# Kernel optimization log

Hardware: AMD Instinct MI355X
Metric: run time of the kernel (lower is better)

Reference implementation:

```python
import jax, jax.numpy as jnp
import numpy as np

# graph metadata: 3 node types, 4 canonical etypes
NT_SRC = (0, 1, 1, 2)   # src ntype of each relation
NT_DST = (1, 0, 2, 1)   # dst ntype of each relation
GROUPS = {0: (1,), 1: (0, 3), 2: (2,)}  # relations sharing each dst ntype (in dict order)
NEG_SLOPE = 0.2
N_NODES, N_EDGES, IN_DIM = 50000, 200000, 256
HEADS, HID = 8, 32
REL_IN, REL_HID = 64, 32


def _leaky(x):
    return jax.nn.leaky_relu(x, NEG_SLOPE)


def _segment_softmax(e, seg, n):
    # numerically stable softmax over edges grouped by dst node
    m = jax.ops.segment_max(e, seg, num_segments=n)
    ex = jnp.exp(e - m[seg])
    s = jax.ops.segment_sum(ex, seg, num_segments=n)
    return ex / s[seg]


def setup_inputs() -> dict:
    key = jax.random.key(0)
    ks = jax.random.split(key, 12)
    w = 0.05  # xavier-like scale
    feat = jax.random.normal(ks[0], (4, N_NODES, IN_DIM), jnp.float32)
    rel_emb = jax.random.normal(ks[1], (4, REL_IN), jnp.float32)
    node_W = jax.random.normal(ks[2], (3, IN_DIM, HEADS * HID), jnp.float32) * w
    rel_W = jax.random.normal(ks[3], (4, REL_IN, HEADS * 2 * HID), jnp.float32) * w
    res_W = jax.random.normal(ks[4], (3, IN_DIM, HEADS * HID), jnp.float32) * w
    res_b = jnp.zeros((3, HEADS * HID), jnp.float32)
    res_alpha = jax.random.normal(ks[5], (3,), jnp.float32)
    cross_attn = jax.random.normal(ks[6], (4, HEADS, HID), jnp.float32) * w
    prop_W = jax.random.normal(ks[7], (4, REL_IN, HEADS * REL_HID), jnp.float32) * w
    prop_b = jnp.zeros((4, HEADS * REL_HID), jnp.float32)
    src_idx = jax.random.randint(ks[8], (4, N_EDGES), 0, N_NODES, jnp.int32)
    dst_idx = jax.random.randint(ks[9], (4, N_EDGES), 0, N_NODES, jnp.int32)
    return dict(feat=feat, rel_emb=rel_emb, node_W=node_W, rel_W=rel_W,
                res_W=res_W, res_b=res_b, res_alpha=res_alpha,
                cross_attn=cross_attn, prop_W=prop_W, prop_b=prop_b,
                src_idx=src_idx, dst_idx=dst_idx)


def reference(feat, rel_emb, node_W, rel_W, res_W, res_b, res_alpha,
              cross_attn, prop_W, prop_b, src_idx, dst_idx):
    R, N, _ = feat.shape
    H, D = HEADS, HID
    conv_out = []
    for r in range(R):  # fixed small set of relations
        s, d = NT_SRC[r], NT_DST[r]
        # RelationGraphConv (dropout is identity in eval)
        fsrc = (feat[r] @ node_W[s]).reshape(N, H, D)
        fdst = (feat[r] @ node_W[d]).reshape(N, H, D)
        ra = (rel_emb[r] @ rel_W[r]).reshape(H, 2 * D)
        e_dst = (fdst * ra[:, :D]).sum(-1)           # (N, H)
        e_src = (fsrc * ra[:, D:]).sum(-1)           # (N, H)
        e = _leaky(e_src[src_idx[r]] + e_dst[dst_idx[r]])  # (E, H)
        a = _segment_softmax(e, dst_idx[r], N)       # edge softmax per dst node
        msg = fsrc[src_idx[r]] * a[:, :, None]       # (E, H, D)
        out = jax.ops.segment_sum(msg, dst_idx[r], num_segments=N)
        out = jax.nn.relu(out.reshape(N, H * D))
        # residual gate
        alpha = jax.nn.sigmoid(res_alpha[d])
        out = out * alpha + (feat[r] @ res_W[d] + res_b[d]) * (1.0 - alpha)
        conv_out.append(out)
    # RelationCrossing over relations sharing the dst ntype
    node_out = []
    for r in range(R):
        group = GROUPS[NT_DST[r]]
        if len(group) == 1:
            node_out.append(conv_out[group[0]])
        else:
            stacked = jnp.stack([conv_out[g] for g in group], 0).reshape(len(group), N, H, D)
            att = _leaky((stacked * cross_attn[r]).sum(-1, keepdims=True))  # (Rg, N, H, 1)
            att = jax.nn.softmax(att, axis=0)
            node_out.append((stacked * att).sum(0).reshape(N, H * D))
    node_out = jnp.stack(node_out, 0)                # (4, N, H*D)
    # relation embedding propagation
    rel_out = jnp.einsum('ri,rio->ro', rel_emb, prop_W) + prop_b  # (4, H*rel_hid)
    return node_out, rel_out
```

## Files before the change

kernel.cpp:

```cpp
#include <hip/hip_runtime.h>
#include <hip/hip_bf16.h>
#include <stdint.h>

typedef unsigned int u32;
typedef unsigned short u16;
typedef short short8 __attribute__((ext_vector_type(8)));
typedef float f32x4 __attribute__((ext_vector_type(4)));
typedef unsigned short u16x4 __attribute__((ext_vector_type(4)));
typedef __attribute__((address_space(1))) const u32 gu32;
typedef __attribute__((address_space(3))) u32 lu32;

#define NN 50000
#define NE 200000
#define WCT 576

__device__ __forceinline__ float leaky(float x){ return x >= 0.f ? x : 0.2f*x; }
__device__ __forceinline__ float bf2f(u16 u){ return __uint_as_float(((u32)u)<<16); }
__device__ __forceinline__ u16 f2bf(float f){
    u32 u = __float_as_uint(f);
    u32 r = (u + 0x7fffu + ((u>>16)&1u)) >> 16;
    return (u16)r;
}
__device__ __forceinline__ u32 pack_bf2(float a, float b){
    return __builtin_amdgcn_perm(__float_as_uint(b), __float_as_uint(a), 0x07060302u);
}
__device__ __forceinline__ int nt_src(int r){ return (r==0)?0:((r==3)?2:1); }
__device__ __forceinline__ int nt_dst(int r){ return (r==1)?0:((r==2)?2:1); }

__global__ void k_ra(const float* __restrict__ rel_emb, const float* __restrict__ rel_W,
                     float* __restrict__ ra){
    int r = blockIdx.x;
    for (int j = threadIdx.x; j < 512; j += blockDim.x){
        float acc = 0.f;
        for (int i = 0; i < 64; i++) acc += rel_emb[r*64+i] * rel_W[(r*64+i)*512 + j];
        ra[r*512 + j] = acc;
    }
}

__global__ void k_wcat(const float* __restrict__ node_W, const float* __restrict__ res_W,
                       const float* __restrict__ ra, u16* __restrict__ WcatS){
    int g = blockIdx.x*blockDim.x + threadIdx.x;
    if (g >= 4*WCT*256) return;
    int r = g/147456; int rem = g%147456;
    int tile = rem/16384; int rem2 = rem%16384;
    int kc = rem2/512; int rem3 = rem2%512;
    int nrow = rem3>>3; int off = rem3&7;
    int n = tile*64 + nrow;
    int k = kc*8 + off;
    int s = nt_src(r), d = nt_dst(r);
    float v;
    if (n < 256) v = node_W[(s*256+k)*256 + n];
    else if (n < 512) v = res_W[(d*256+k)*256 + (n-256)];
    else if (n < 520){
        int h = n-512; float a = 0.f;
        for (int dd = 0; dd < 32; dd++) a += node_W[(s*256+k)*256 + h*32+dd] * ra[r*512 + h*64+32+dd];
        v = a;
    } else if (n < 528){
        int h = n-520; float a = 0.f;
        for (int dd = 0; dd < 32; dd++) a += node_W[(d*256+k)*256 + h*32+dd] * ra[r*512 + h*64+dd];
        v = a;
    } else v = 0.f;
    WcatS[g] = f2bf(v);
}

__launch_bounds__(512, 4)
__global__ void k_gemm(const float* __restrict__ feat, const u16* __restrict__ WcatS,
                       const float* __restrict__ res_b,
                       u16* __restrict__ fsrc, u16* __restrict__ resb,
                       float* __restrict__ e_comb){
    __shared__ uint4 lsB[4096];
    const short8* lsB8 = (const short8*)lsB;

    int r = blockIdx.y;
    int row0 = blockIdx.x*128;
    const float* A = feat + (size_t)r*NN*256;
    const u16*   W = WcatS + (size_t)r*9*16384;

    int t = threadIdx.x;
    int w = t>>6, l = t&63;
    int wm = (w>>1)*32, wn = (w&1)*32;
    int li = l & 15, lg = l >> 4;

    short8 afr[2][8];
    #pragma unroll
    for (int mt = 0; mt < 2; mt++){
        int grow = row0 + wm + mt*16 + li; if (grow > NN-1) grow = NN-1;
        const float* ap = A + (size_t)grow*256 + lg*8;
        #pragma unroll
        for (int kk = 0; kk < 8; kk++){
            f32x4 x = __builtin_nontemporal_load((const f32x4*)(ap + kk*32));
            f32x4 y = __builtin_nontemporal_load((const f32x4*)(ap + kk*32 + 4));
            short8 f;
            ((u32*)&f)[0] = pack_bf2(x.x, x.y);
            ((u32*)&f)[1] = pack_bf2(x.z, x.w);
            ((u32*)&f)[2] = pack_bf2(y.x, y.y);
            ((u32*)&f)[3] = pack_bf2(y.z, y.w);
            afr[mt][kk] = f;
        }
    }

    #pragma unroll
    for (int i = 0; i < 4; i++){
        int chunk = i*512 + t;
        __builtin_amdgcn_global_load_lds((gu32*)(W + (size_t)chunk*8),
                                         (lu32*)((char*)lsB + chunk*16), 16, 0, 0);
    }
    __syncthreads();

    int d = nt_dst(r);
    int orow = t>>2, oq = t&3;
    int ogrow = row0 + orow;
    size_t onidx = (size_t)r*NN + ogrow;

    for (int T = 0; T < 8; T++){
        int cur = T & 1;
        {
            const u16* tb = W + (size_t)(T+1)*16384;
            char* lb = (char*)lsB + (cur^1)*32768;
            #pragma unroll
            for (int i = 0; i < 4; i++){
                int chunk = i*512 + t;
                __builtin_amdgcn_global_load_lds((gu32*)(tb + (size_t)chunk*8),
                                                 (lu32*)(lb + chunk*16), 16, 0, 0);
            }
        }
        f32x4 acc[2][2] = {};
        #pragma unroll
        for (int kk = 0; kk < 8; kk++){
            short8 bfr[2];
            #pragma unroll
            for (int nt = 0; nt < 2; nt++)
                bfr[nt] = lsB8[cur*2048 + (kk*4+lg)*64 + wn + nt*16 + li];
            #pragma unroll
            for (int mt = 0; mt < 2; mt++)
                #pragma unroll
                for (int nt = 0; nt < 2; nt++)
                    acc[mt][nt] = __builtin_amdgcn_mfma_f32_16x16x32_bf16(afr[mt][kk], bfr[nt], acc[mt][nt], 0,0,0);
        }
        float bias[2] = {0.f, 0.f};
        if (T >= 4){
            bias[0] = res_b[d*256 + (T-4)*64 + wn + li];
            bias[1] = res_b[d*256 + (T-4)*64 + wn + 16 + li];
        }
        __syncthreads();
        u16* cst = (u16*)(lsB + (size_t)cur*2048);
        #pragma unroll
        for (int mt = 0; mt < 2; mt++)
            #pragma unroll
            for (int nt = 0; nt < 2; nt++)
                #pragma unroll
                for (int qq = 0; qq < 4; qq++)
                    cst[(wm + mt*16 + lg*4 + qq)*72 + wn + nt*16 + li] = f2bf(acc[mt][nt][qq] + bias[nt]);
        __syncthreads();
        if (ogrow < NN){
            u16* dst = (T < 4) ? (fsrc + onidx*256 + T*64) : (resb + onidx*256 + (T-4)*64);
            const uint4* src = (const uint4*)(cst + orow*72 + oq*16);
            uint4* dq = (uint4*)(dst + oq*16);
            dq[0] = src[0];
            dq[1] = src[1];
        }
        __syncthreads();
    }

    if (wn == 0){
        f32x4 acc[2] = {};
        #pragma unroll
        for (int kk = 0; kk < 8; kk++){
            short8 bfr = lsB8[(kk*4+lg)*64 + li];
            #pragma unroll
            for (int mt = 0; mt < 2; mt++)
                acc[mt] = __builtin_amdgcn_mfma_f32_16x16x32_bf16(afr[mt][kk], bfr, acc[mt], 0,0,0);
        }
        #pragma unroll
        for (int mt = 0; mt < 2; mt++)
            #pragma unroll
            for (int qq = 0; qq < 4; qq++){
                int row = row0 + wm + mt*16 + lg*4 + qq;
                if (row < NN)
                    e_comb[((size_t)r*NN + row)*16 + li] = acc[mt][qq];
            }
    }
}


__global__ void k_count(const int* __restrict__ dst_idx, u32* __restrict__ cnt){
    int r = blockIdx.y; int e = blockIdx.x*256 + threadIdx.x;
    if (e >= NE) return;
    atomicAdd(&cnt[r*NN + dst_idx[r*NE+e]], 1u);
}

__global__ void k_scan1(const u32* __restrict__ cnt, u32* __restrict__ bsum){
    int r = blockIdx.y, b = blockIdx.x;
    int i = b*256 + threadIdx.x;
    u32 v = (i < NN) ? cnt[r*NN+i] : 0u;
    #pragma unroll
    for (int off = 1; off < 64; off <<= 1) v += __shfl_xor(v, off, 64);
    __shared__ u32 wsum[4];
    int lane = threadIdx.x & 63, w = threadIdx.x >> 6;
    if (lane == 0) wsum[w] = v;
    __syncthreads();
    if (threadIdx.x == 0) bsum[r*256 + b] = wsum[0]+wsum[1]+wsum[2]+wsum[3];
}

__device__ __forceinline__ u32 block_scan_incl(u32 v){
    __shared__ u32 wsum[4];
    int lane = threadIdx.x & 63, w = threadIdx.x >> 6;
    #pragma unroll
    for (int off = 1; off < 64; off <<= 1){
        u32 t = __shfl_up(v, off, 64);
        if (lane >= off) v += t;
    }
    if (lane == 63) wsum[w] = v;
    __syncthreads();
    u32 add = 0;
    #pragma unroll
    for (int k = 0; k < 4; k++) if (k < w) add += wsum[k];
    return v + add;
}

__global__ void k_scan2(u32* __restrict__ bsum){
    int r = blockIdx.x;
    u32 v = bsum[r*256 + threadIdx.x];
    u32 incl = block_scan_incl(v);
    bsum[r*256 + threadIdx.x] = incl - v;
}

__global__ void k_scan3(const u32* __restrict__ cnt, const u32* __restrict__ bsum,
                        u32* __restrict__ row_ptr){
    int r = blockIdx.y, b = blockIdx.x;
    int i = b*256 + threadIdx.x;
    u32 v = (i < NN) ? cnt[r*NN+i] : 0u;
    u32 incl = block_scan_incl(v);
    if (i < NN) row_ptr[r*(NN+1) + i + 1] = bsum[r*256 + b] + incl;
    if (b == 0 && threadIdx.x == 0) row_ptr[r*(NN+1)] = 0u;
}

__global__ void k_scatter(const int* __restrict__ src_idx, const int* __restrict__ dst_idx,
                          const float* __restrict__ e_comb,
                          const u32* __restrict__ row_ptr, u32* __restrict__ cnt2,
                          u32* __restrict__ src_pack, float* __restrict__ e_pack){
    int r = blockIdx.y; int e = blockIdx.x*256 + threadIdx.x;
    if (e >= NE) return;
    int s = src_idx[r*NE+e], d = dst_idx[r*NE+e];
    u32 pos = row_ptr[r*(NN+1)+d] + atomicAdd(&cnt2[r*NN+d], 1u);
    src_pack[r*NE + pos] = (u32)s;
    const f32x4* es = (const f32x4*)(e_comb + (size_t)(r*NN+s)*16);
    const f32x4* ed = (const f32x4*)(e_comb + (size_t)(r*NN+d)*16 + 8);
    f32x4 s0 = es[0], s1 = es[1], d0 = ed[0], d1 = ed[1];
    f32x4 w0, w1;
    w0.x = __expf(leaky(s0.x+d0.x)); w0.y = __expf(leaky(s0.y+d0.y));
    w0.z = __expf(leaky(s0.z+d0.z)); w0.w = __expf(leaky(s0.w+d0.w));
    w1.x = __expf(leaky(s1.x+d1.x)); w1.y = __expf(leaky(s1.y+d1.y));
    w1.z = __expf(leaky(s1.z+d1.z)); w1.w = __expf(leaky(s1.w+d1.w));
    f32x4* ep = (f32x4*)(e_pack + ((size_t)(r*NE)+pos)*8);
    ep[0] = w0; ep[1] = w1;
}

__device__ __forceinline__ void agg_core(int n, int r, int l, int h,
                                         const u32* __restrict__ row_ptr,
                                         const u32* __restrict__ src_pack,
                                         const float* __restrict__ e_pack,
                                         const u16* __restrict__ fsrc,
                                         const u16* __restrict__ resb,
                                         const float* __restrict__ res_alpha,
                                         float& c0, float& c1, float& c2, float& c3){
    u32 p0 = row_ptr[r*(NN+1)+n];
    u32 p1 = row_ptr[r*(NN+1)+n+1];
    int deg = (int)(p1 - p0);

    float s = 0.f;
    for (int i = (l>>3); i < deg; i += 8)
        s += e_pack[((size_t)(r*NE) + p0 + i)*8 + (l&7)];
    #pragma unroll
    for (int msk = 8; msk < 64; msk <<= 1)
        s += __shfl_xor(s, msk, 64);
    float sh = __shfl(s, h, 64);
    float inv_sh = (deg > 0) ? 1.0f / sh : 0.f;

    float a0=0.f, a1=0.f, a2=0.f, a3=0.f;
    const size_t ebase = (size_t)r*NE + p0;
    const u16* fbase = fsrc + (size_t)r*NN*256;
    for (int base = 0; base < deg; base += 64){
        int rem = deg - base; if (rem > 64) rem = 64;
        u32 my_src = 0;
        if (l < rem) my_src = src_pack[ebase + base + l];
        int i = 0;
        for (; i+4 <= rem; i += 4){
            u32 s0 = __shfl(my_src, i, 64);
            u32 s1 = __shfl(my_src, i+1, 64);
            u32 s2 = __shfl(my_src, i+2, 64);
            u32 s3 = __shfl(my_src, i+3, 64);
            float ex0 = e_pack[(ebase + base + i)*8 + h];
            float ex1 = e_pack[(ebase + base + i + 1)*8 + h];
            float ex2 = e_pack[(ebase + base + i + 2)*8 + h];
            float ex3 = e_pack[(ebase + base + i + 3)*8 + h];
            ushort4 f0 = *(const ushort4*)(fbase + (size_t)s0*256 + l*4);
            ushort4 f1 = *(const ushort4*)(fbase + (size_t)s1*256 + l*4);
            ushort4 f2 = *(const ushort4*)(fbase + (size_t)s2*256 + l*4);
            ushort4 f3 = *(const ushort4*)(fbase + (size_t)s3*256 + l*4);
            float w0 = ex0*inv_sh, w1 = ex1*inv_sh, w2 = ex2*inv_sh, w3 = ex3*inv_sh;
            a0 += bf2f(f0.x)*w0 + bf2f(f1.x)*w1 + bf2f(f2.x)*w2 + bf2f(f3.x)*w3;
            a1 += bf2f(f0.y)*w0 + bf2f(f1.y)*w1 + bf2f(f2.y)*w2 + bf2f(f3.y)*w3;
            a2 += bf2f(f0.z)*w0 + bf2f(f1.z)*w1 + bf2f(f2.z)*w2 + bf2f(f3.z)*w3;
            a3 += bf2f(f0.w)*w0 + bf2f(f1.w)*w1 + bf2f(f2.w)*w2 + bf2f(f3.w)*w3;
        }
        for (; i < rem; i++){
            u32 s0 = __shfl(my_src, i, 64);
            float w0 = e_pack[(ebase + base + i)*8 + h]*inv_sh;
            ushort4 f0 = *(const ushort4*)(fbase + (size_t)s0*256 + l*4);
            a0 += bf2f(f0.x)*w0; a1 += bf2f(f0.y)*w0; a2 += bf2f(f0.z)*w0; a3 += bf2f(f0.w)*w0;
        }
    }

    int d = nt_dst(r);
    float alpha = 1.f/(1.f + __expf(-res_alpha[d]));
    float beta = 1.f - alpha;
    u16x4 rv = __builtin_nontemporal_load((const u16x4*)(resb + ((size_t)r*NN+n)*256 + l*4));
    c0 = fmaxf(a0,0.f)*alpha + bf2f(rv.x)*beta;
    c1 = fmaxf(a1,0.f)*alpha + bf2f(rv.y)*beta;
    c2 = fmaxf(a2,0.f)*alpha + bf2f(rv.z)*beta;
    c3 = fmaxf(a3,0.f)*alpha + bf2f(rv.w)*beta;
}

__launch_bounds__(128)
__global__ void k_agg12(const u32* __restrict__ row_ptr, const u32* __restrict__ src_pack,
                        const float* __restrict__ e_pack, const u16* __restrict__ fsrc,
                        const u16* __restrict__ resb, const float* __restrict__ res_alpha,
                        float* __restrict__ out){
    int n = blockIdx.x;
    int r = 1 + (threadIdx.x >> 6);
    int l = threadIdx.x & 63;
    int h = l >> 3;
    float c0, c1, c2, c3;
    agg_core(n, r, l, h, row_ptr, src_pack, e_pack, fsrc, resb, res_alpha, c0, c1, c2, c3);
    f32x4 o = {c0, c1, c2, c3};
    __builtin_nontemporal_store(o, (f32x4*)(out + ((size_t)r*NN+n)*256 + l*4));
}

__launch_bounds__(128)
__global__ void k_aggx03(const u32* __restrict__ row_ptr, const u32* __restrict__ src_pack,
                         const float* __restrict__ e_pack, const u16* __restrict__ fsrc,
                         const u16* __restrict__ resb, const float* __restrict__ res_alpha,
                         const float* __restrict__ cross_attn, float* __restrict__ out){
    __shared__ float cbuf[2][256];
    __shared__ float dots[4][8];

    int n = blockIdx.x;
    int w = threadIdx.x >> 6;
    int r = w ? 3 : 0;
    int l = threadIdx.x & 63;
    int h = l >> 3;
    float c0, c1, c2, c3;
    agg_core(n, r, l, h, row_ptr, src_pack, e_pack, fsrc, resb, res_alpha, c0, c1, c2, c3);

    int slot = w;
    cbuf[slot][l*4+0] = c0; cbuf[slot][l*4+1] = c1;
    cbuf[slot][l*4+2] = c2; cbuf[slot][l*4+3] = c3;
    const float* ca0 = cross_attn;
    const float* ca3 = cross_attn + 3*256;
    float d0 = c0*ca0[l*4+0] + c1*ca0[l*4+1] + c2*ca0[l*4+2] + c3*ca0[l*4+3];
    float d3 = c0*ca3[l*4+0] + c1*ca3[l*4+1] + c2*ca3[l*4+2] + c3*ca3[l*4+3];
    #pragma unroll
    for (int msk = 1; msk < 8; msk <<= 1){
        d0 += __shfl_xor(d0, msk, 64);
        d3 += __shfl_xor(d3, msk, 64);
    }
    if ((l & 7) == 0){
        dots[slot*2+0][h] = d0;
        dots[slot*2+1][h] = d3;
    }
    __syncthreads();
    float g0 = (r == 0) ? dots[0][h] : dots[1][h];
    float g3 = (r == 0) ? dots[2][h] : dots[3][h];
    g0 = leaky(g0); g3 = leaky(g3);
    float mm = fmaxf(g0, g3);
    float w0 = __expf(g0-mm), w3 = __expf(g3-mm);
    float inv = 1.f/(w0+w3);
    w0 *= inv; w3 *= inv;
    f32x4 o;
    o.x = w0*cbuf[0][l*4+0] + w3*cbuf[1][l*4+0];
    o.y = w0*cbuf[0][l*4+1] + w3*cbuf[1][l*4+1];
    o.z = w0*cbuf[0][l*4+2] + w3*cbuf[1][l*4+2];
    o.w = w0*cbuf[0][l*4+3] + w3*cbuf[1][l*4+3];
    __builtin_nontemporal_store(o, (f32x4*)(out + ((size_t)r*NN+n)*256 + l*4));
}

__global__ void k_relout(const float* __restrict__ rel_emb, const float* __restrict__ prop_W,
                         const float* __restrict__ prop_b, float* __restrict__ out){
    int r = blockIdx.x; int o = threadIdx.x;
    float acc = prop_b[r*256 + o];
    for (int i = 0; i < 64; i++) acc += rel_emb[r*64+i] * prop_W[(r*64+i)*256 + o];
    out[(size_t)4*NN*256 + r*256 + o] = acc;
}

extern "C" void kernel_launch(void* const* d_in, const int* in_sizes, int n_in,
                              void* d_out, int out_size, void* d_ws, size_t ws_size,
                              hipStream_t stream){
    const float* feat      = (const float*)d_in[0];
    const float* rel_emb   = (const float*)d_in[1];
    const float* node_W    = (const float*)d_in[2];
    const float* rel_W     = (const float*)d_in[3];
    const float* res_W     = (const float*)d_in[4];
    const float* res_b     = (const float*)d_in[5];
    const float* res_alpha = (const float*)d_in[6];
    const float* cross_attn= (const float*)d_in[7];
    const float* prop_W    = (const float*)d_in[8];
    const float* prop_b    = (const float*)d_in[9];
    const int* src_idx     = (const int*)d_in[10];
    const int* dst_idx     = (const int*)d_in[11];
    float* out = (float*)d_out;

    char* ws = (char*)d_ws;
    u32*   cnt     = (u32*)  (ws);
    u32*   cnt2    = (u32*)  (ws + 800000);
    u32*   bsum    = (u32*)  (ws + 1600000);
    u32*   row_ptr = (u32*)  (ws + 1604096);
    float* ra      = (float*)(ws + 2404112);
    u16*   WcatS   = (u16*)  (ws + 2412304);
    float* e_comb  = (float*)(ws + 3591952);
    u32*   src_pack= (u32*)  (ws + 16391952);
    float* e_pack  = (float*)(ws + 19591952);
    u16*   fsrc    = (u16*)  (ws + 45191952);
    u16*   resb    = (u16*)  (ws + 147591952);

    hipMemsetAsync(cnt, 0, 1604096, stream);

    k_ra<<<4, 256, 0, stream>>>(rel_emb, rel_W, ra);
    k_wcat<<<(4*WCT*256)/256, 256, 0, stream>>>(node_W, res_W, ra, WcatS);
    dim3 gg((NN+127)/128, 4);
    k_gemm<<<gg, 512, 0, stream>>>(feat, WcatS, res_b, fsrc, resb, e_comb);

    dim3 geg((NE+255)/256, 4);
    k_count<<<geg, 256, 0, stream>>>(dst_idx, cnt);
    dim3 gsc((NN+255)/256, 4);
    k_scan1<<<gsc, 256, 0, stream>>>(cnt, bsum);
    k_scan2<<<4, 256, 0, stream>>>(bsum);
    k_scan3<<<gsc, 256, 0, stream>>>(cnt, bsum, row_ptr);
    k_scatter<<<geg, 256, 0, stream>>>(src_idx, dst_idx, e_comb, row_ptr, cnt2,
                                       src_pack, e_pack);
    k_agg12<<<NN, 128, 0, stream>>>(row_ptr, src_pack, e_pack, fsrc, resb,
                                    res_alpha, out);
    k_aggx03<<<NN, 128, 0, stream>>>(row_ptr, src_pack, e_pack, fsrc, resb,
                                     res_alpha, cross_attn, out);
    k_relout<<<4, 256, 0, stream>>>(rel_emb, prop_W, prop_b, out);
}
```

Baseline: 428.1 us.

## Split aggregation into per-relation launches and store GEMM outputs directly

Aggregation now runs as one launch per relation, with four destination nodes per 256-thread block, instead of mixing two relations per 128-thread block. This keeps each relation's gathered feature table hot in cache and removes the LDS exchange and barrier from the cross-relation step. Relation 0's result goes to a bf16 scratch buffer that reuses relation 1's freed fsrc slot, and the final kernel mixes it with relation 3. That adds an extra write and read and bf16 rounding of an intermediate. Separately, the GEMM epilogue writes bf16 results straight to global memory rather than staging them through LDS, which drops two barriers per tile but makes the stores narrower and strided.

```diff
diff --git a/kernel.cpp b/kernel.cpp
--- a/kernel.cpp
+++ b/kernel.cpp
@@ -108,10 +108,6 @@
     __syncthreads();
 
     int d = nt_dst(r);
-    int orow = t>>2, oq = t&3;
-    int ogrow = row0 + orow;
-    size_t onidx = (size_t)r*NN + ogrow;
-
     for (int T = 0; T < 8; T++){
         int cur = T & 1;
         {
@@ -143,23 +139,19 @@
             bias[1] = res_b[d*256 + (T-4)*64 + wn + 16 + li];
         }
         __syncthreads();
-        u16* cst = (u16*)(lsB + (size_t)cur*2048);
+        u16* base = (T < 4) ? fsrc : resb;
+        int cb = (T & 3)*64 + wn;
         #pragma unroll
         for (int mt = 0; mt < 2; mt++)
             #pragma unroll
-            for (int nt = 0; nt < 2; nt++)
-                #pragma unroll
-                for (int qq = 0; qq < 4; qq++)
-                    cst[(wm + mt*16 + lg*4 + qq)*72 + wn + nt*16 + li] = f2bf(acc[mt][nt][qq] + bias[nt]);
-        __syncthreads();
-        if (ogrow < NN){
-            u16* dst = (T < 4) ? (fsrc + onidx*256 + T*64) : (resb + onidx*256 + (T-4)*64);
-            const uint4* src = (const uint4*)(cst + orow*72 + oq*16);
-            uint4* dq = (uint4*)(dst + oq*16);
-            dq[0] = src[0];
-            dq[1] = src[1];
-        }
-        __syncthreads();
+            for (int qq = 0; qq < 4; qq++){
+                int row = row0 + wm + mt*16 + lg*4 + qq;
+                if (row < NN){
+                    size_t off = ((size_t)r*NN + row)*256 + cb;
+                    base[off + li]      = f2bf(acc[mt][0][qq] + bias[0]);
+                    base[off + 16 + li] = f2bf(acc[mt][1][qq] + bias[1]);
+                }
+            }
     }
 
     if (wn == 0){
@@ -322,67 +314,76 @@
     c3 = fmaxf(a3,0.f)*alpha + bf2f(rv.w)*beta;
 }
 
-__launch_bounds__(128)
-__global__ void k_agg12(const u32* __restrict__ row_ptr, const u32* __restrict__ src_pack,
-                        const float* __restrict__ e_pack, const u16* __restrict__ fsrc,
-                        const u16* __restrict__ resb, const float* __restrict__ res_alpha,
-                        float* __restrict__ out){
-    int n = blockIdx.x;
-    int r = 1 + (threadIdx.x >> 6);
+__launch_bounds__(256)
+__global__ void k_aggr(const u32* __restrict__ row_ptr, const u32* __restrict__ src_pack,
+                       const float* __restrict__ e_pack, const u16* __restrict__ fsrc,
+                       const u16* __restrict__ resb, const float* __restrict__ res_alpha,
+                       float* __restrict__ out, int r){
+    int n = blockIdx.x*4 + (threadIdx.x >> 6);
+    if (n >= NN) return;
+    int l = threadIdx.x & 63;
+    float c0, c1, c2, c3;
+    agg_core(n, r, l, l>>3, row_ptr, src_pack, e_pack, fsrc, resb, res_alpha, c0, c1, c2, c3);
+    f32x4 o = {c0, c1, c2, c3};
+    __builtin_nontemporal_store(o, (f32x4*)(out + ((size_t)r*NN+n)*256 + l*4));
+}
+
+__launch_bounds__(256)
+__global__ void k_aggA(const u32* __restrict__ row_ptr, const u32* __restrict__ src_pack,
+                       const float* __restrict__ e_pack, const u16* __restrict__ fsrc,
+                       const u16* __restrict__ resb, const float* __restrict__ res_alpha,
+                       u16* __restrict__ tmp0){
+    int n = blockIdx.x*4 + (threadIdx.x >> 6);
+    if (n >= NN) return;
+    int l = threadIdx.x & 63;
+    float c0, c1, c2, c3;
+    agg_core(n, 0, l, l>>3, row_ptr, src_pack, e_pack, fsrc, resb, res_alpha, c0, c1, c2, c3);
+    u16x4 o = {f2bf(c0), f2bf(c1), f2bf(c2), f2bf(c3)};
+    *(u16x4*)(tmp0 + (size_t)n*256 + l*4) = o;
+}
+
+__launch_bounds__(256)
+__global__ void k_aggB(const u32* __restrict__ row_ptr, const u32* __restrict__ src_pack,
+                       const float* __restrict__ e_pack, const u16* __restrict__ fsrc,
+                       const u16* __restrict__ resb, const float* __restrict__ res_alpha,
+                       const u16* __restrict__ tmp0, const float* __restrict__ cross_attn,
+                       float* __restrict__ out){
+    int n = blockIdx.x*4 + (threadIdx.x >> 6);
+    if (n >= NN) return;
     int l = threadIdx.x & 63;
     int h = l >> 3;
-    float c0, c1, c2, c3;
-    agg_core(n, r, l, h, row_ptr, src_pack, e_pack, fsrc, resb, res_alpha, c0, c1, c2, c3);
-    f32x4 o = {c0, c1, c2, c3};
-    __builtin_nontemporal_store(o, (f32x4*)(out + ((size_t)r*NN+n)*256 + l*4));
-}
-
-__launch_bounds__(128)
-__global__ void k_aggx03(const u32* __restrict__ row_ptr, const u32* __restrict__ src_pack,
-                         const float* __restrict__ e_pack, const u16* __restrict__ fsrc,
-                         const u16* __restrict__ resb, const float* __restrict__ res_alpha,
-                         const float* __restrict__ cross_attn, float* __restrict__ out){
-    __shared__ float cbuf[2][256];
-    __shared__ float dots[4][8];
-
-    int n = blockIdx.x;
-    int w = threadIdx.x >> 6;
-    int r = w ? 3 : 0;
-    int l = threadIdx.x & 63;
-    int h = l >> 3;
-    float c0, c1, c2, c3;
-    agg_core(n, r, l, h, row_ptr, src_pack, e_pack, fsrc, resb, res_alpha, c0, c1, c2, c3);
-
-    int slot = w;
-    cbuf[slot][l*4+0] = c0; cbuf[slot][l*4+1] = c1;
-    cbuf[slot][l*4+2] = c2; cbuf[slot][l*4+3] = c3;
+    float b0, b1, b2, b3;
+    agg_core(n, 3, l, h, row_ptr, src_pack, e_pack, fsrc, resb, res_alpha, b0, b1, b2, b3);
+    u16x4 tv = *(const u16x4*)(tmp0 + (size_t)n*256 + l*4);
+    float a0 = bf2f(tv.x), a1 = bf2f(tv.y), a2 = bf2f(tv.z), a3 = bf2f(tv.w);
+
     const float* ca0 = cross_attn;
     const float* ca3 = cross_attn + 3*256;
-    float d0 = c0*ca0[l*4+0] + c1*ca0[l*4+1] + c2*ca0[l*4+2] + c3*ca0[l*4+3];
-    float d3 = c0*ca3[l*4+0] + c1*ca3[l*4+1] + c2*ca3[l*4+2] + c3*ca3[l*4+3];
+    float w00 = a0*ca0[l*4+0] + a1*ca0[l*4+1] + a2*ca0[l*4+2] + a3*ca0[l*4+3];
+    float w30 = b0*ca0[l*4+0] + b1*ca0[l*4+1] + b2*ca0[l*4+2] + b3*ca0[l*4+3];
+    float w03 = a0*ca3[l*4+0] + a1*ca3[l*4+1] + a2*ca3[l*4+2] + a3*ca3[l*4+3];
+    float w33 = b0*ca3[l*4+0] + b1*ca3[l*4+1] + b2*ca3[l*4+2] + b3*ca3[l*4+3];
     #pragma unroll
     for (int msk = 1; msk < 8; msk <<= 1){
-        d0 += __shfl_xor(d0, msk, 64);
-        d3 += __shfl_xor(d3, msk, 64);
-    }
-    if ((l & 7) == 0){
-        dots[slot*2+0][h] = d0;
-        dots[slot*2+1][h] = d3;
-    }
-    __syncthreads();
-    float g0 = (r == 0) ? dots[0][h] : dots[1][h];
-    float g3 = (r == 0) ? dots[2][h] : dots[3][h];
-    g0 = leaky(g0); g3 = leaky(g3);
+        w00 += __shfl_xor(w00, msk, 64);
+        w30 += __shfl_xor(w30, msk, 64);
+        w03 += __shfl_xor(w03, msk, 64);
+        w33 += __shfl_xor(w33, msk, 64);
+    }
+    float g0 = leaky(w00), g3 = leaky(w30);
     float mm = fmaxf(g0, g3);
-    float w0 = __expf(g0-mm), w3 = __expf(g3-mm);
-    float inv = 1.f/(w0+w3);
-    w0 *= inv; w3 *= inv;
-    f32x4 o;
-    o.x = w0*cbuf[0][l*4+0] + w3*cbuf[1][l*4+0];
-    o.y = w0*cbuf[0][l*4+1] + w3*cbuf[1][l*4+1];
-    o.z = w0*cbuf[0][l*4+2] + w3*cbuf[1][l*4+2];
-    o.w = w0*cbuf[0][l*4+3] + w3*cbuf[1][l*4+3];
-    __builtin_nontemporal_store(o, (f32x4*)(out + ((size_t)r*NN+n)*256 + l*4));
+    float e0 = __expf(g0-mm), e3 = __expf(g3-mm);
+    float inv = 1.f/(e0+e3);
+    float u0 = e0*inv, u3 = e3*inv;
+    f32x4 o0 = {u0*a0 + u3*b0, u0*a1 + u3*b1, u0*a2 + u3*b2, u0*a3 + u3*b3};
+    __builtin_nontemporal_store(o0, (f32x4*)(out + (size_t)n*256 + l*4));
+    float q0 = leaky(w03), q3 = leaky(w33);
+    float mq = fmaxf(q0, q3);
+    float v0 = __expf(q0-mq), v3 = __expf(q3-mq);
+    float iv = 1.f/(v0+v3);
+    v0 *= iv; v3 *= iv;
+    f32x4 o3 = {v0*a0 + v3*b0, v0*a1 + v3*b1, v0*a2 + v3*b2, v0*a3 + v3*b3};
+    __builtin_nontemporal_store(o3, (f32x4*)(out + ((size_t)3*NN+n)*256 + l*4));
 }
 
 __global__ void k_relout(const float* __restrict__ rel_emb, const float* __restrict__ prop_W,
@@ -422,6 +423,7 @@
     float* e_pack  = (float*)(ws + 19591952);
     u16*   fsrc    = (u16*)  (ws + 45191952);
     u16*   resb    = (u16*)  (ws + 147591952);
+    u16*   tmp0    = fsrc + (size_t)NN*256;
 
     hipMemsetAsync(cnt, 0, 1604096, stream);
 
@@ -438,9 +440,11 @@
     k_scan3<<<gsc, 256, 0, stream>>>(cnt, bsum, row_ptr);
     k_scatter<<<geg, 256, 0, stream>>>(src_idx, dst_idx, e_comb, row_ptr, cnt2,
                                        src_pack, e_pack);
-    k_agg12<<<NN, 128, 0, stream>>>(row_ptr, src_pack, e_pack, fsrc, resb,
-                                    res_alpha, out);
-    k_aggx03<<<NN, 128, 0, stream>>>(row_ptr, src_pack, e_pack, fsrc, resb,
-                                     res_alpha, cross_attn, out);
+    int gag = (NN+3)/4;
+    k_aggr<<<gag, 256, 0, stream>>>(row_ptr, src_pack, e_pack, fsrc, resb, res_alpha, out, 1);
+    k_aggr<<<gag, 256, 0, stream>>>(row_ptr, src_pack, e_pack, fsrc, resb, res_alpha, out, 2);
+    k_aggA<<<gag, 256, 0, stream>>>(row_ptr, src_pack, e_pack, fsrc, resb, res_alpha, tmp0);
+    k_aggB<<<gag, 256, 0, stream>>>(row_ptr, src_pack, e_pack, fsrc, resb, res_alpha,
+                                    tmp0, cross_attn, out);
     k_relout<<<4, 256, 0, stream>>>(rel_emb, prop_W, prop_b, out);
 }
```

Measured after the change: 453.8 us. +6.0%, slower.

## Write GEMM outputs directly from registers and pad node stride to remove syncs

Applied to the files above, without the earlier changes.

The GEMM epilogue no longer stages bf16 results through LDS with three block barriers per tile. Each lane now stores its accumulator values straight to global memory, using a padded per-relation row stride (NNP) so the bounds checks can go. The first weight tile load is issued before the A-fragment loads, biases are preloaded once, and the T loop is unrolled with manual vmcnt waits and a single barrier per iteration. In exchange, global stores become narrow 2-byte scattered writes instead of coalesced 16-byte rows, and the workspace layout grows. Correctness also depends on the hand-tuned s_waitcnt counts.

```diff
diff --git a/kernel.cpp b/kernel.cpp
--- a/kernel.cpp
+++ b/kernel.cpp
@@ -11,6 +11,7 @@
 typedef __attribute__((address_space(3))) u32 lu32;
 
 #define NN 50000
+#define NNP 50048
 #define NE 200000
 #define WCT 576
 
@@ -81,6 +82,13 @@
     int wm = (w>>1)*32, wn = (w&1)*32;
     int li = l & 15, lg = l >> 4;
 
+    #pragma unroll
+    for (int i = 0; i < 4; i++){
+        int chunk = i*512 + t;
+        __builtin_amdgcn_global_load_lds((gu32*)(W + (size_t)chunk*8),
+                                         (lu32*)((char*)lsB + chunk*16), 16, 0, 0);
+    }
+
     short8 afr[2][8];
     #pragma unroll
     for (int mt = 0; mt < 2; mt++){
@@ -99,19 +107,20 @@
         }
     }
 
-    #pragma unroll
-    for (int i = 0; i < 4; i++){
-        int chunk = i*512 + t;
-        __builtin_amdgcn_global_load_lds((gu32*)(W + (size_t)chunk*8),
-                                         (lu32*)((char*)lsB + chunk*16), 16, 0, 0);
-    }
-    __syncthreads();
-
     int d = nt_dst(r);
-    int orow = t>>2, oq = t&3;
-    int ogrow = row0 + orow;
-    size_t onidx = (size_t)r*NN + ogrow;
-
+    float bias0[4], bias1[4];
+    #pragma unroll
+    for (int j = 0; j < 4; j++){
+        bias0[j] = res_b[d*256 + j*64 + wn + li];
+        bias1[j] = res_b[d*256 + j*64 + wn + 16 + li];
+        asm volatile("" : "+v"(bias0[j]), "+v"(bias1[j]));
+    }
+
+    asm volatile("s_waitcnt vmcnt(0)" ::: "memory");
+    __builtin_amdgcn_sched_barrier(0);
+    __builtin_amdgcn_s_barrier();
+
+    #pragma unroll
     for (int T = 0; T < 8; T++){
         int cur = T & 1;
         {
@@ -124,6 +133,7 @@
                                                  (lu32*)(lb + chunk*16), 16, 0, 0);
             }
         }
+        __builtin_amdgcn_sched_barrier(0);
         f32x4 acc[2][2] = {};
         #pragma unroll
         for (int kk = 0; kk < 8; kk++){
@@ -137,29 +147,22 @@
                 for (int nt = 0; nt < 2; nt++)
                     acc[mt][nt] = __builtin_amdgcn_mfma_f32_16x16x32_bf16(afr[mt][kk], bfr[nt], acc[mt][nt], 0,0,0);
         }
-        float bias[2] = {0.f, 0.f};
-        if (T >= 4){
-            bias[0] = res_b[d*256 + (T-4)*64 + wn + li];
-            bias[1] = res_b[d*256 + (T-4)*64 + wn + 16 + li];
-        }
-        __syncthreads();
-        u16* cst = (u16*)(lsB + (size_t)cur*2048);
+        u16* base = (T < 4) ? fsrc : resb;
+        int cb = (T & 3)*64 + wn;
+        float b0 = (T >= 4) ? bias0[T-4] : 0.f;
+        float b1 = (T >= 4) ? bias1[T-4] : 0.f;
         #pragma unroll
         for (int mt = 0; mt < 2; mt++)
             #pragma unroll
-            for (int nt = 0; nt < 2; nt++)
-                #pragma unroll
-                for (int qq = 0; qq < 4; qq++)
-                    cst[(wm + mt*16 + lg*4 + qq)*72 + wn + nt*16 + li] = f2bf(acc[mt][nt][qq] + bias[nt]);
-        __syncthreads();
-        if (ogrow < NN){
-            u16* dst = (T < 4) ? (fsrc + onidx*256 + T*64) : (resb + onidx*256 + (T-4)*64);
-            const uint4* src = (const uint4*)(cst + orow*72 + oq*16);
-            uint4* dq = (uint4*)(dst + oq*16);
-            dq[0] = src[0];
-            dq[1] = src[1];
-        }
-        __syncthreads();
+            for (int qq = 0; qq < 4; qq++){
+                int row = row0 + wm + mt*16 + lg*4 + qq;
+                size_t off = ((size_t)r*NNP + row)*256 + cb;
+                base[off + li]      = f2bf(acc[mt][0][qq] + b0);
+                base[off + 16 + li] = f2bf(acc[mt][1][qq] + b1);
+            }
+        asm volatile("s_waitcnt vmcnt(16)" ::: "memory");
+        __builtin_amdgcn_sched_barrier(0);
+        __builtin_amdgcn_s_barrier();
     }
 
     if (wn == 0){
@@ -176,8 +179,7 @@
             #pragma unroll
             for (int qq = 0; qq < 4; qq++){
                 int row = row0 + wm + mt*16 + lg*4 + qq;
-                if (row < NN)
-                    e_comb[((size_t)r*NN + row)*16 + li] = acc[mt][qq];
+                e_comb[((size_t)r*NNP + row)*16 + li] = acc[mt][qq];
             }
     }
 }
@@ -244,8 +246,8 @@
     int s = src_idx[r*NE+e], d = dst_idx[r*NE+e];
     u32 pos = row_ptr[r*(NN+1)+d] + atomicAdd(&cnt2[r*NN+d], 1u);
     src_pack[r*NE + pos] = (u32)s;
-    const f32x4* es = (const f32x4*)(e_comb + (size_t)(r*NN+s)*16);
-    const f32x4* ed = (const f32x4*)(e_comb + (size_t)(r*NN+d)*16 + 8);
+    const f32x4* es = (const f32x4*)(e_comb + ((size_t)r*NNP + s)*16);
+    const f32x4* ed = (const f32x4*)(e_comb + ((size_t)r*NNP + d)*16 + 8);
     f32x4 s0 = es[0], s1 = es[1], d0 = ed[0], d1 = ed[1];
     f32x4 w0, w1;
     w0.x = __expf(leaky(s0.x+d0.x)); w0.y = __expf(leaky(s0.y+d0.y));
@@ -279,7 +281,7 @@
 
     float a0=0.f, a1=0.f, a2=0.f, a3=0.f;
     const size_t ebase = (size_t)r*NE + p0;
-    const u16* fbase = fsrc + (size_t)r*NN*256;
+    const u16* fbase = fsrc + (size_t)r*NNP*256;
     for (int base = 0; base < deg; base += 64){
         int rem = deg - base; if (rem > 64) rem = 64;
         u32 my_src = 0;
@@ -315,7 +317,7 @@
     int d = nt_dst(r);
     float alpha = 1.f/(1.f + __expf(-res_alpha[d]));
     float beta = 1.f - alpha;
-    u16x4 rv = __builtin_nontemporal_load((const u16x4*)(resb + ((size_t)r*NN+n)*256 + l*4));
+    u16x4 rv = __builtin_nontemporal_load((const u16x4*)(resb + ((size_t)r*NNP+n)*256 + l*4));
     c0 = fmaxf(a0,0.f)*alpha + bf2f(rv.x)*beta;
     c1 = fmaxf(a1,0.f)*alpha + bf2f(rv.y)*beta;
     c2 = fmaxf(a2,0.f)*alpha + bf2f(rv.z)*beta;
@@ -418,16 +420,16 @@
     float* ra      = (float*)(ws + 2404112);
     u16*   WcatS   = (u16*)  (ws + 2412304);
     float* e_comb  = (float*)(ws + 3591952);
-    u32*   src_pack= (u32*)  (ws + 16391952);
-    float* e_pack  = (float*)(ws + 19591952);
-    u16*   fsrc    = (u16*)  (ws + 45191952);
-    u16*   resb    = (u16*)  (ws + 147591952);
+    u32*   src_pack= (u32*)  (ws + 16404240);
+    float* e_pack  = (float*)(ws + 19604240);
+    u16*   fsrc    = (u16*)  (ws + 45204240);
+    u16*   resb    = (u16*)  (ws + 147702544);
 
     hipMemsetAsync(cnt, 0, 1604096, stream);
 
     k_ra<<<4, 256, 0, stream>>>(rel_emb, rel_W, ra);
     k_wcat<<<(4*WCT*256)/256, 256, 0, stream>>>(node_W, res_W, ra, WcatS);
-    dim3 gg((NN+127)/128, 4);
+    dim3 gg(NNP/128, 4);
     k_gemm<<<gg, 512, 0, stream>>>(feat, WcatS, res_b, fsrc, resb, e_comb);
 
     dim3 geg((NE+255)/256, 4);
```

Measured after the change: 473.2 us. 1.11x slower.
